# Kernel optimization log

Measured on AMD Instinct MI355X. Metric: run time of the kernel, lower is better.

## Reference

```python
import jax, jax.numpy as jnp
import numpy as np


def setup_inputs() -> dict:
    key = jax.random.key(0)
    ks = jax.random.split(key, 8)
    B, T, D, H, HD = 4, 2048, 1024, 16, 64
    s = 0.02
    return {
        "x": jax.random.normal(ks[0], (B, T, D), dtype=jnp.float32),
        "Wq": jax.random.normal(ks[1], (H, D, HD), dtype=jnp.float32) * s,
        "bq": jnp.zeros((H, HD), dtype=jnp.float32),
        "Wk": jax.random.normal(ks[2], (H, D, HD), dtype=jnp.float32) * s,
        "bk": jnp.zeros((H, HD), dtype=jnp.float32),
        "Wv": jax.random.normal(ks[3], (H, D, HD), dtype=jnp.float32) * s,
        "bv": jnp.zeros((H, HD), dtype=jnp.float32),
        "Wo": jax.random.normal(ks[4], (D, D), dtype=jnp.float32) * s,
        "bo": jnp.zeros((D,), dtype=jnp.float32),
        "mask": 1,
    }


def reference(x, Wq, bq, Wk, bk, Wv, bv, Wo, bo, mask):
    B, T, D = x.shape
    # stacked per-head projections: [B,H,T,hd]
    q = jnp.einsum('btd,hde->bhte', x, Wq) + bq[None, :, None, :]
    k = jnp.einsum('btd,hde->bhte', x, Wk) + bk[None, :, None, :]
    v = jnp.einsum('btd,hde->bhte', x, Wv) + bv[None, :, None, :]
    hd = q.shape[-1]
    # FAITHFUL to source: scores = QK^T / hd**(-0.5) == QK^T * sqrt(hd)
    scores = jnp.einsum('bhte,bhse->bhts', q, k) * (float(hd) ** 0.5)
    if mask:
        causal = jnp.tril(jnp.ones((T, T), dtype=bool))
        scores = jnp.where(causal[None, None, :, :], scores, -jnp.inf)
    att = jax.nn.softmax(scores, axis=-1)  # dropout is identity in eval
    out = jnp.einsum('bhts,bhse->bhte', att, v)
    # concat heads along feature dim (head order matches ModuleList order)
    out = out.transpose(0, 2, 1, 3).reshape(B, T, D)
    return out @ Wo + bo
```

## Files before the change

### kernel.cpp

```cpp
#include <hip/hip_runtime.h>
#include <hip/hip_bf16.h>
#include <math.h>

#define B_  4
#define T_  2048
#define D_  1024
#define H_  16
#define HD_ 64
#define M_  8192

typedef __attribute__((ext_vector_type(8))) _Float16 f16x8;
typedef __attribute__((ext_vector_type(4))) float   f32x4;

static __device__ __forceinline__ unsigned short f2h(float f){
    union { _Float16 h; unsigned short u; } cv; cv.h = (_Float16)f; return cv.u;
}
static __device__ __forceinline__ void gload_lds16(const void* g, void* l){
    __builtin_amdgcn_global_load_lds(
        (const __attribute__((address_space(1))) unsigned int*)g,
        (__attribute__((address_space(3))) unsigned int*)l, 16, 0, 0);
}

union U16x16 { unsigned short us[16]; uint4 q[2]; };
union U16x4  { unsigned short us[4];  uint2 q;    };

__global__ __launch_bounds__(256) void prep_xh(
    const float* __restrict__ x, unsigned short* __restrict__ xb)
{
    const size_t i = ((size_t)blockIdx.x*256 + threadIdx.x)*16;
    U16x16 u;
#pragma unroll
    for (int j=0;j<16;j+=4){
        float4 f = *(const float4*)(x+i+j);
        u.us[j+0]=f2h(f.x); u.us[j+1]=f2h(f.y);
        u.us[j+2]=f2h(f.z); u.us[j+3]=f2h(f.w);
    }
    *(uint4*)(xb+i)   = u.q[0];
    *(uint4*)(xb+i+8) = u.q[1];
}

__global__ __launch_bounds__(256) void prep_wqkvh(
    const float* __restrict__ Wq, const float* __restrict__ Wk,
    const float* __restrict__ Wv, unsigned short* __restrict__ wt)
{
    const int dt = blockIdx.x;
    const int zh = blockIdx.y;
    const int z = zh >> 4, h = zh & 15;
    const float* src = ((z==0)?Wq:(z==1)?Wk:Wv) + (size_t)h*1024*64;
    __shared__ float Tt[64][68];
    const int t = threadIdx.x;
    const int r = t >> 2, c4 = (t & 3) * 16;
    const float* sp = src + (size_t)(dt*64 + r)*64 + c4;
    float4 v0=*(const float4*)(sp+0), v1=*(const float4*)(sp+4);
    float4 v2=*(const float4*)(sp+8), v3=*(const float4*)(sp+12);
    *(float4*)&Tt[r][c4+ 0]=v0; *(float4*)&Tt[r][c4+ 4]=v1;
    *(float4*)&Tt[r][c4+ 8]=v2; *(float4*)&Tt[r][c4+12]=v3;
    __syncthreads();
    const int er = t >> 2, dk = (t & 3) * 16;
    U16x16 u;
#pragma unroll
    for (int j=0;j<16;j++) u.us[j] = f2h(Tt[dk+j][er]);
    unsigned short* dst = wt + (size_t)(z*1024 + h*64 + er)*1024 + dt*64 + dk;
    *(uint4*)(dst)   = u.q[0];
    *(uint4*)(dst+8) = u.q[1];
}

__global__ __launch_bounds__(256) void prep_woh(
    const float* __restrict__ Wo, unsigned short* __restrict__ wot)
{
    const int kt = blockIdx.x, nt = blockIdx.y;
    __shared__ float Tt[64][68];
    const int t = threadIdx.x;
    const int r = t >> 2, c4 = (t & 3) * 16;
    const float* sp = Wo + (size_t)(kt*64 + r)*1024 + nt*64 + c4;
    float4 v0=*(const float4*)(sp+0), v1=*(const float4*)(sp+4);
    float4 v2=*(const float4*)(sp+8), v3=*(const float4*)(sp+12);
    *(float4*)&Tt[r][c4+ 0]=v0; *(float4*)&Tt[r][c4+ 4]=v1;
    *(float4*)&Tt[r][c4+ 8]=v2; *(float4*)&Tt[r][c4+12]=v3;
    __syncthreads();
    const int er = t >> 2, dk = (t & 3) * 16;
    U16x16 u;
#pragma unroll
    for (int j=0;j<16;j++) u.us[j] = f2h(Tt[dk+j][er]);
    unsigned short* dst = wot + (size_t)(nt*64 + er)*1024 + kt*64 + dk;
    *(uint4*)(dst)   = u.q[0];
    *(uint4*)(dst+8) = u.q[1];
}

__global__ __launch_bounds__(256) void gemm_qkvh(
    const unsigned short* __restrict__ xb, const unsigned short* __restrict__ wt,
    const float* __restrict__ bqv, const float* __restrict__ bkv,
    const float* __restrict__ bvv,
    unsigned short* __restrict__ qp, unsigned short* __restrict__ kp,
    unsigned short* __restrict__ vtp)
{
    const int m0 = blockIdx.x * 128;
    const int n0 = blockIdx.y * 128;
    const int tid = threadIdx.x;
    const int lane = tid & 63, w = tid >> 6;
    const int wr = w >> 1, wc = w & 1;
    const int fla = lane & 15, flb = lane >> 4;

    __shared__ unsigned short As[128*32];
    __shared__ unsigned short Bs[128*32];

    f32x4 acc[4][4];
#pragma unroll
    for (int i=0;i<4;i++)
#pragma unroll
        for (int j=0;j<4;j++) acc[i][j] = (f32x4){0.f,0.f,0.f,0.f};

    const int srow0 = w*32 + (lane>>2);
    const int srow1 = srow0 + 16;
    const int spc   = lane & 3;
    const size_t ga0 = (size_t)(m0+srow0)*1024 + (size_t)((spc ^ ((srow0>>1)&3))*8);
    const size_t ga1 = (size_t)(m0+srow1)*1024 + (size_t)((spc ^ ((srow1>>1)&3))*8);
    const size_t gb0 = (size_t)(n0+srow0)*1024 + (size_t)((spc ^ ((srow0>>1)&3))*8);
    const size_t gb1 = (size_t)(n0+srow1)*1024 + (size_t)((spc ^ ((srow1>>1)&3))*8);
    const int ldso0 = w*1024;
    const int ldso1 = w*1024 + 512;
    const int pchunk = (flb ^ ((fla>>1)&3)) * 8;

    for (int ks = 0; ks < 32; ++ks){
        const size_t k0 = (size_t)ks*32;
        __syncthreads();
        gload_lds16(xb + ga0 + k0, As + ldso0);
        gload_lds16(xb + ga1 + k0, As + ldso1);
        gload_lds16(wt + gb0 + k0, Bs + ldso0);
        gload_lds16(wt + gb1 + k0, Bs + ldso1);
        __syncthreads();

        f16x8 af[4], bfr[4];
#pragma unroll
        for (int mf=0; mf<4; ++mf)
            af[mf] = *(const f16x8*)&As[(wr*64+mf*16+fla)*32 + pchunk];
#pragma unroll
        for (int nf=0; nf<4; ++nf)
            bfr[nf] = *(const f16x8*)&Bs[(wc*64+nf*16+fla)*32 + pchunk];
#pragma unroll
        for (int mf=0; mf<4; ++mf)
#pragma unroll
            for (int nf=0; nf<4; ++nf)
                acc[mf][nf] = __builtin_amdgcn_mfma_f32_16x16x32_f16(
                                  af[mf], bfr[nf], acc[mf][nf], 0, 0, 0);
    }

#pragma unroll
    for (int nf=0; nf<4; ++nf){
        const int c = n0 + wc*64 + nf*16 + fla;
        const int z = c >> 10, rem = c & 1023;
        const int h = rem >> 6, e = rem & 63;
        if (z < 2){
            const float bias = ((z==0)?bqv:bkv)[rem];
            const float scl  = (z==0) ? 11.541560327111708f
                                      : 1.0f;
            unsigned short* op = (z==0)?qp:kp;
#pragma unroll
            for (int mf=0; mf<4; ++mf){
#pragma unroll
                for (int ri=0; ri<4; ++ri){
                    const int m = m0 + wr*64 + mf*16 + flb*4 + ri;
                    const int b = m >> 11, t = m & (T_-1);
                    op[((size_t)(b*H_ + h)*T_ + t)*HD_ + e] =
                        f2h((acc[mf][nf][ri] + bias) * scl);
                }
            }
        } else {
            const float bias = bvv[rem];
#pragma unroll
            for (int mf=0; mf<4; ++mf){
                const int m = m0 + wr*64 + mf*16 + flb*4;
                const int b = m >> 11, t = m & (T_-1);
                U16x4 u;
#pragma unroll
                for (int ri=0; ri<4; ++ri)
                    u.us[ri] = f2h(acc[mf][nf][ri] + bias);
                *(uint2*)(vtp + ((size_t)(b*H_ + h)*HD_ + e)*T_ + t) = u.q;
            }
        }
    }
}

__global__ __launch_bounds__(256) void gemm_o(
    const unsigned short* __restrict__ attb, const unsigned short* __restrict__ wot,
    const float* __restrict__ bo, float* __restrict__ out)
{
    const int m0 = blockIdx.x * 128;
    const int n0 = blockIdx.y * 128;
    const int tid = threadIdx.x;
    const int lane = tid & 63, w = tid >> 6;
    const int wr = w >> 1, wc = w & 1;
    const int fla = lane & 15, flb = lane >> 4;

    __shared__ unsigned short As[4096];
    __shared__ unsigned short Bs[4096];

    f32x4 acc[4][4];
#pragma unroll
    for (int i=0;i<4;i++)
#pragma unroll
        for (int j=0;j<4;j++) acc[i][j] = (f32x4){0.f,0.f,0.f,0.f};

    const int srow0 = w*32 + (lane>>2);
    const int srow1 = srow0 + 16;
    const int spc   = lane & 3;
    const size_t ga0 = (size_t)(m0+srow0)*1024 + (size_t)((spc ^ ((srow0>>1)&3))*8);
    const size_t ga1 = (size_t)(m0+srow1)*1024 + (size_t)((spc ^ ((srow1>>1)&3))*8);
    const size_t gb0 = (size_t)(n0+srow0)*1024 + (size_t)((spc ^ ((srow0>>1)&3))*8);
    const size_t gb1 = (size_t)(n0+srow1)*1024 + (size_t)((spc ^ ((srow1>>1)&3))*8);
    const int ldso0 = w*1024;
    const int ldso1 = w*1024 + 512;
    const int pchunk = (flb ^ ((fla>>1)&3)) * 8;

    for (int ks = 0; ks < 32; ++ks){
        const size_t k0 = (size_t)ks*32;
        __syncthreads();
        gload_lds16(attb + ga0 + k0, As + ldso0);
        gload_lds16(attb + ga1 + k0, As + ldso1);
        gload_lds16(wot  + gb0 + k0, Bs + ldso0);
        gload_lds16(wot  + gb1 + k0, Bs + ldso1);
        __syncthreads();

        f16x8 af[4], bfr[4];
#pragma unroll
        for (int mf=0; mf<4; ++mf)
            af[mf] = *(const f16x8*)&As[(wr*64+mf*16+fla)*32 + pchunk];
#pragma unroll
        for (int nf=0; nf<4; ++nf)
            bfr[nf] = *(const f16x8*)&Bs[(wc*64+nf*16+fla)*32 + pchunk];
#pragma unroll
        for (int mf=0; mf<4; ++mf)
#pragma unroll
            for (int nf=0; nf<4; ++nf)
                acc[mf][nf] = __builtin_amdgcn_mfma_f32_16x16x32_f16(
                                  af[mf], bfr[nf], acc[mf][nf], 0, 0, 0);
    }

#pragma unroll
    for (int nf=0; nf<4; ++nf){
        const int n = n0 + wc*64 + nf*16 + fla;
        const float bias = bo[n];
#pragma unroll
        for (int mf=0; mf<4; ++mf){
#pragma unroll
            for (int ri=0; ri<4; ++ri){
                const int m = m0 + wr*64 + mf*16 + flb*4 + ri;
                out[(size_t)m*D_ + n] = acc[mf][nf][ri] + bias;
            }
        }
    }
}

__global__ __launch_bounds__(256) void attn_mfma(
    const unsigned short* __restrict__ qp, const unsigned short* __restrict__ kp,
    const unsigned short* __restrict__ vtp, unsigned short* __restrict__ attb,
    const int* __restrict__ maskp)
{
    const int bid = blockIdx.x;
    const int qb  = 31 - (bid >> 6);
    const int bh  = bid & 63;
    const int b   = bh >> 4, h = bh & 15;
    const int tid = threadIdx.x;
    const int lane = tid & 63, w = tid >> 6;
    const int l16 = lane & 15, h16 = lane >> 4;
    const int domask = maskp[0];

    __shared__ unsigned short KS [2][128][32];
    __shared__ unsigned short VtS[4][64][32];
    __shared__ unsigned short PsS[4][64][32];

    const int qrow = qb*64 + w*16 + l16;
    const size_t qoff = ((size_t)bh*T_ + qrow)*HD_ + 8*h16;
    const f16x8 q0 = *(const f16x8*)(qp + qoff);
    const f16x8 q1 = *(const f16x8*)(qp + qoff + 32);

    f32x4 accO[4];
#pragma unroll
    for (int j=0;j<4;j++) accO[j] = (f32x4){0.f,0.f,0.f,0.f};
    float m_run[4], lpart[4];
#pragma unroll
    for (int i=0;i<4;i++){ m_run[i] = -INFINITY; lpart[i] = 0.f; }

    const int kr = tid >> 1;
    const int kh = tid & 1;
    const int fk = (kr >> 1) & 3;
    const int vr = tid >> 2;
    const int vq = tid & 3;
    const int fv = (vr >> 1) & 3;

    const int off = (h16 ^ ((l16>>1)&3)) * 8;

    const size_t kbase = (size_t)bh*T_*HD_;
    const size_t vbase = (size_t)bh*HD_*T_;

    const int nchunks = domask ? ((qb+2)>>1) : 16;
    for (int ci = 0; ci < nchunks; ++ci){
        const int kb = ci << 7;
        const unsigned short* ksrc = kp + kbase + (size_t)(kb+kr)*HD_ + kh*32;
        uint4 ka0=*(const uint4*)(ksrc),    ka1=*(const uint4*)(ksrc+8);
        uint4 ka2=*(const uint4*)(ksrc+16), ka3=*(const uint4*)(ksrc+24);
        const unsigned short* vsrc = vtp + vbase + (size_t)vr*T_ + kb + vq*32;
        uint4 va0=*(const uint4*)(vsrc),    va1=*(const uint4*)(vsrc+8);
        uint4 va2=*(const uint4*)(vsrc+16), va3=*(const uint4*)(vsrc+24);
        __syncthreads();
        *(uint4*)&KS [kh][kr][(0^fk)*8] = ka0;
        *(uint4*)&KS [kh][kr][(1^fk)*8] = ka1;
        *(uint4*)&KS [kh][kr][(2^fk)*8] = ka2;
        *(uint4*)&KS [kh][kr][(3^fk)*8] = ka3;
        *(uint4*)&VtS[vq][vr][(0^fv)*8] = va0;
        *(uint4*)&VtS[vq][vr][(1^fv)*8] = va1;
        *(uint4*)&VtS[vq][vr][(2^fv)*8] = va2;
        *(uint4*)&VtS[vq][vr][(3^fv)*8] = va3;
        __syncthreads();

        f32x4 s[8];
#pragma unroll
        for (int j=0;j<8;j++){
            const f16x8 k0 = *(const f16x8*)&KS[0][j*16+l16][off];
            const f16x8 k1 = *(const f16x8*)&KS[1][j*16+l16][off];
            f32x4 a = (f32x4){0.f,0.f,0.f,0.f};
            a = __builtin_amdgcn_mfma_f32_16x16x32_f16(q0, k0, a, 0,0,0);
            a = __builtin_amdgcn_mfma_f32_16x16x32_f16(q1, k1, a, 0,0,0);
            s[j] = a;
        }
        if (domask && ci == nchunks-1){
#pragma unroll
            for (int j=0;j<8;j++)
#pragma unroll
                for (int reg=0;reg<4;reg++)
                    if (kb + j*16 + l16 > qb*64 + w*16 + h16*4 + reg)
                        s[j][reg] = -INFINITY;
        }

        float pmax[4];
#pragma unroll
        for (int reg=0; reg<4; ++reg){
            float m0 = fmaxf(fmaxf(s[0][reg],s[1][reg]), fmaxf(s[2][reg],s[3][reg]));
            float m1 = fmaxf(fmaxf(s[4][reg],s[5][reg]), fmaxf(s[6][reg],s[7][reg]));
            float mloc = fmaxf(m0, m1);
            mloc = fmaxf(mloc, __shfl_xor(mloc,1));
            mloc = fmaxf(mloc, __shfl_xor(mloc,2));
            mloc = fmaxf(mloc, __shfl_xor(mloc,4));
            mloc = fmaxf(mloc, __shfl_xor(mloc,8));
            pmax[reg] = mloc;
        }
        const bool small = (pmax[0] <= m_run[0]+8.f) && (pmax[1] <= m_run[1]+8.f)
                        && (pmax[2] <= m_run[2]+8.f) && (pmax[3] <= m_run[3]+8.f);
        if (!__all(small)){
#pragma unroll
            for (int reg=0; reg<4; ++reg){
                const float mnew = fmaxf(m_run[reg], pmax[reg]);
                const float scl  = exp2f(m_run[reg] - mnew);
                m_run[reg] = mnew;
                lpart[reg] *= scl;
                accO[0][reg] *= scl; accO[1][reg] *= scl;
                accO[2][reg] *= scl; accO[3][reg] *= scl;
            }
        }

        const int sblo = l16 >> 3, pos = l16 & 7;
#pragma unroll
        for (int reg=0; reg<4; ++reg){
            const float mr = m_run[reg];
            const int prow = w*16 + h16*4 + reg;
            const int psw  = (prow>>1)&3;
            float ps = 0.f;
#pragma unroll
            for (int j=0;j<8;j++){
                const float p = exp2f(s[j][reg]-mr);
                ps += p;
                PsS[j>>1][prow][(((j&1)*2 + sblo) ^ psw)*8 + pos] = f2h(p);
            }
            lpart[reg] += ps;
        }

#pragma unroll
        for (int kc=0;kc<4;kc++){
            const f16x8 pa = *(const f16x8*)&PsS[kc][w*16+l16][off];
#pragma unroll
            for (int j=0;j<4;j++){
                const f16x8 vb_ = *(const f16x8*)&VtS[kc][j*16+l16][off];
                accO[j] = __builtin_amdgcn_mfma_f32_16x16x32_f16(pa, vb_, accO[j], 0,0,0);
            }
        }
    }

#pragma unroll
    for (int reg=0;reg<4;reg++){
        float l = lpart[reg];
        l += __shfl_xor(l,1); l += __shfl_xor(l,2);
        l += __shfl_xor(l,4); l += __shfl_xor(l,8);
        const float inv = 1.0f / l;
        const int t = qb*64 + w*16 + h16*4 + reg;
#pragma unroll
        for (int j=0;j<4;j++){
            attb[((size_t)b*T_ + t)*D_ + h*HD_ + j*16 + l16] =
                f2h(accO[j][reg]*inv);
        }
    }
}

extern "C" void kernel_launch(void* const* d_in, const int* in_sizes, int n_in,
                              void* d_out, int out_size, void* d_ws, size_t ws_size,
                              hipStream_t stream)
{
    const float* x  = (const float*)d_in[0];
    const float* Wq = (const float*)d_in[1];
    const float* bq = (const float*)d_in[2];
    const float* Wk = (const float*)d_in[3];
    const float* bk = (const float*)d_in[4];
    const float* Wv = (const float*)d_in[5];
    const float* bv = (const float*)d_in[6];
    const float* Wo = (const float*)d_in[7];
    const float* bo = (const float*)d_in[8];
    const int* mask = (const int*)d_in[9];
    float* out = (float*)d_out;

    unsigned short* qp  = (unsigned short*)d_ws;
    unsigned short* kp  = qp  + (size_t)8*1024*1024;
    unsigned short* vtp = kp  + (size_t)8*1024*1024;
    unsigned short* xb  = vtp + (size_t)8*1024*1024;
    unsigned short* wt  = xb  + (size_t)8*1024*1024;
    unsigned short* wot = wt  + (size_t)3*1024*1024;
    unsigned short* attb = xb;

    prep_xh   <<<2048, 256, 0, stream>>>(x, xb);
    prep_wqkvh<<<dim3(16,48), 256, 0, stream>>>(Wq, Wk, Wv, wt);
    prep_woh  <<<dim3(16,16), 256, 0, stream>>>(Wo, wot);
    gemm_qkvh <<<dim3(64,24), 256, 0, stream>>>(xb, wt, bq, bk, bv, qp, kp, vtp);
    attn_mfma <<<2048, 256, 0, stream>>>(qp, kp, vtp, attb, mask);
    gemm_o    <<<dim3(64,8), 256, 0, stream>>>(attb, wot, bo, out);
}
```

Measured before the change: 203.4 us.

## Compute transposed S tile so each lane owns one query row in softmax

Swaps the MFMA operands so the score tile comes out transposed: each lane holds one query row across four key columns. The row max and sum then need only two cross-lane shuffles instead of four per register, and the running max and sum become scalars per lane. P is written to shared memory as packed half2 values via cvt_pkrtz instead of single halves. The rescale and final normalisation factors are redistributed to the accumulator layout with extra shuffles. The pkrtz conversion rounds toward zero rather than to nearest.

Result: faster. 189.1 us (-7.0%).

```diff
diff --git a/kernel.cpp b/kernel.cpp
--- a/kernel.cpp
+++ b/kernel.cpp
@@ -10,10 +10,16 @@
 #define M_  8192
 
 typedef __attribute__((ext_vector_type(8))) _Float16 f16x8;
+typedef __attribute__((ext_vector_type(2))) __fp16  h16x2;
 typedef __attribute__((ext_vector_type(4))) float   f32x4;
 
 static __device__ __forceinline__ unsigned short f2h(float f){
     union { _Float16 h; unsigned short u; } cv; cv.h = (_Float16)f; return cv.u;
+}
+static __device__ __forceinline__ unsigned int pkh2(float a, float b){
+    union { h16x2 h; unsigned int u; } cv;
+    cv.h = __builtin_amdgcn_cvt_pkrtz(a, b);
+    return cv.u;
 }
 static __device__ __forceinline__ void gload_lds16(const void* g, void* l){
     __builtin_amdgcn_global_load_lds(
@@ -277,9 +283,7 @@
     f32x4 accO[4];
 #pragma unroll
     for (int j=0;j<4;j++) accO[j] = (f32x4){0.f,0.f,0.f,0.f};
-    float m_run[4], lpart[4];
-#pragma unroll
-    for (int i=0;i<4;i++){ m_run[i] = -INFINITY; lpart[i] = 0.f; }
+    float m_run = -INFINITY, lpart = 0.f;
 
     const int kr = tid >> 1;
     const int kh = tid & 1;
@@ -289,6 +293,7 @@
     const int fv = (vr >> 1) & 3;
 
     const int off = (h16 ^ ((l16>>1)&3)) * 8;
+    const int psw = (l16>>1)&3;
 
     const size_t kbase = (size_t)bh*T_*HD_;
     const size_t vbase = (size_t)bh*HD_*T_;
@@ -319,8 +324,8 @@
             const f16x8 k0 = *(const f16x8*)&KS[0][j*16+l16][off];
             const f16x8 k1 = *(const f16x8*)&KS[1][j*16+l16][off];
             f32x4 a = (f32x4){0.f,0.f,0.f,0.f};
-            a = __builtin_amdgcn_mfma_f32_16x16x32_f16(q0, k0, a, 0,0,0);
-            a = __builtin_amdgcn_mfma_f32_16x16x32_f16(q1, k1, a, 0,0,0);
+            a = __builtin_amdgcn_mfma_f32_16x16x32_f16(k0, q0, a, 0,0,0);
+            a = __builtin_amdgcn_mfma_f32_16x16x32_f16(k1, q1, a, 0,0,0);
             s[j] = a;
         }
         if (domask && ci == nchunks-1){
@@ -328,51 +333,57 @@
             for (int j=0;j<8;j++)
 #pragma unroll
                 for (int reg=0;reg<4;reg++)
-                    if (kb + j*16 + l16 > qb*64 + w*16 + h16*4 + reg)
+                    if (kb + j*16 + 4*h16 + reg > qrow)
                         s[j][reg] = -INFINITY;
         }
 
-        float pmax[4];
-#pragma unroll
-        for (int reg=0; reg<4; ++reg){
-            float m0 = fmaxf(fmaxf(s[0][reg],s[1][reg]), fmaxf(s[2][reg],s[3][reg]));
-            float m1 = fmaxf(fmaxf(s[4][reg],s[5][reg]), fmaxf(s[6][reg],s[7][reg]));
-            float mloc = fmaxf(m0, m1);
-            mloc = fmaxf(mloc, __shfl_xor(mloc,1));
-            mloc = fmaxf(mloc, __shfl_xor(mloc,2));
-            mloc = fmaxf(mloc, __shfl_xor(mloc,4));
-            mloc = fmaxf(mloc, __shfl_xor(mloc,8));
-            pmax[reg] = mloc;
-        }
-        const bool small = (pmax[0] <= m_run[0]+8.f) && (pmax[1] <= m_run[1]+8.f)
-                        && (pmax[2] <= m_run[2]+8.f) && (pmax[3] <= m_run[3]+8.f);
+        float mx01 = fmaxf(fmaxf(s[0][0],s[0][1]), fmaxf(s[0][2],s[0][3]));
+        float mx1  = fmaxf(fmaxf(s[1][0],s[1][1]), fmaxf(s[1][2],s[1][3]));
+        float mx2  = fmaxf(fmaxf(s[2][0],s[2][1]), fmaxf(s[2][2],s[2][3]));
+        float mx3  = fmaxf(fmaxf(s[3][0],s[3][1]), fmaxf(s[3][2],s[3][3]));
+        float mx4  = fmaxf(fmaxf(s[4][0],s[4][1]), fmaxf(s[4][2],s[4][3]));
+        float mx5  = fmaxf(fmaxf(s[5][0],s[5][1]), fmaxf(s[5][2],s[5][3]));
+        float mx6  = fmaxf(fmaxf(s[6][0],s[6][1]), fmaxf(s[6][2],s[6][3]));
+        float mx7  = fmaxf(fmaxf(s[7][0],s[7][1]), fmaxf(s[7][2],s[7][3]));
+        float mloc = fmaxf(fmaxf(fmaxf(mx01,mx1), fmaxf(mx2,mx3)),
+                           fmaxf(fmaxf(mx4,mx5), fmaxf(mx6,mx7)));
+        mloc = fmaxf(mloc, __shfl_xor(mloc,16));
+        mloc = fmaxf(mloc, __shfl_xor(mloc,32));
+
+        const bool small = (mloc <= m_run + 8.f);
         if (!__all(small)){
-#pragma unroll
-            for (int reg=0; reg<4; ++reg){
-                const float mnew = fmaxf(m_run[reg], pmax[reg]);
-                const float scl  = exp2f(m_run[reg] - mnew);
-                m_run[reg] = mnew;
-                lpart[reg] *= scl;
-                accO[0][reg] *= scl; accO[1][reg] *= scl;
-                accO[2][reg] *= scl; accO[3][reg] *= scl;
+            const float mnew = fmaxf(m_run, mloc);
+            const float scl  = exp2f(m_run - mnew);
+            m_run = mnew;
+            lpart *= scl;
+            const float sr0 = __shfl(scl, 4*h16+0);
+            const float sr1 = __shfl(scl, 4*h16+1);
+            const float sr2 = __shfl(scl, 4*h16+2);
+            const float sr3 = __shfl(scl, 4*h16+3);
+#pragma unroll
+            for (int j=0;j<4;j++){
+                accO[j][0] *= sr0; accO[j][1] *= sr1;
+                accO[j][2] *= sr2; accO[j][3] *= sr3;
             }
         }
 
-        const int sblo = l16 >> 3, pos = l16 & 7;
-#pragma unroll
-        for (int reg=0; reg<4; ++reg){
-            const float mr = m_run[reg];
-            const int prow = w*16 + h16*4 + reg;
-            const int psw  = (prow>>1)&3;
-            float ps = 0.f;
-#pragma unroll
-            for (int j=0;j<8;j++){
-                const float p = exp2f(s[j][reg]-mr);
-                ps += p;
-                PsS[j>>1][prow][(((j&1)*2 + sblo) ^ psw)*8 + pos] = f2h(p);
-            }
-            lpart[reg] += ps;
-        }
+        const int prow = w*16 + l16;
+        float ps = 0.f;
+#pragma unroll
+        for (int j=0;j<8;j++){
+            const float p0 = exp2f(s[j][0]-m_run);
+            const float p1 = exp2f(s[j][1]-m_run);
+            const float p2 = exp2f(s[j][2]-m_run);
+            const float p3 = exp2f(s[j][3]-m_run);
+            ps += (p0+p1)+(p2+p3);
+            const unsigned int u01 = pkh2(p0,p1);
+            const unsigned int u23 = pkh2(p2,p3);
+            const int sb = 2*(j&1) + (h16>>1);
+            const int so = ((sb ^ psw)<<3) + 4*(h16&1);
+            *(unsigned int*)&PsS[j>>1][prow][so]   = u01;
+            *(unsigned int*)&PsS[j>>1][prow][so+2] = u23;
+        }
+        lpart += ps;
 
 #pragma unroll
         for (int kc=0;kc<4;kc++){
@@ -385,18 +396,21 @@
         }
     }
 
-#pragma unroll
-    for (int reg=0;reg<4;reg++){
-        float l = lpart[reg];
-        l += __shfl_xor(l,1); l += __shfl_xor(l,2);
-        l += __shfl_xor(l,4); l += __shfl_xor(l,8);
-        const float inv = 1.0f / l;
-        const int t = qb*64 + w*16 + h16*4 + reg;
-#pragma unroll
-        for (int j=0;j<4;j++){
-            attb[((size_t)b*T_ + t)*D_ + h*HD_ + j*16 + l16] =
-                f2h(accO[j][reg]*inv);
-        }
+    float l = lpart;
+    l += __shfl_xor(l,16); l += __shfl_xor(l,32);
+    const float inv = 1.0f / l;
+    const float ir0 = __shfl(inv, 4*h16+0);
+    const float ir1 = __shfl(inv, 4*h16+1);
+    const float ir2 = __shfl(inv, 4*h16+2);
+    const float ir3 = __shfl(inv, 4*h16+3);
+    const int t0 = qb*64 + w*16 + 4*h16;
+#pragma unroll
+    for (int j=0;j<4;j++){
+        const size_t base = ((size_t)b*T_ + t0)*D_ + h*HD_ + j*16 + l16;
+        attb[base        ] = f2h(accO[j][0]*ir0);
+        attb[base +   D_ ] = f2h(accO[j][1]*ir1);
+        attb[base + 2*D_ ] = f2h(accO[j][2]*ir2);
+        attb[base + 3*D_ ] = f2h(accO[j][3]*ir3);
     }
 }
 
```
